# Optimization experiments

Measured on AMD Instinct MI355X. Metric: run time of the kernel, lower is better.

Reference implementation:

```python
import jax, jax.numpy as jnp
import numpy as np

K = 1024  # num_embeddings
D = 256   # embedding_dim
COMMIT = 0.25

def setup_inputs() -> dict:
    key = jax.random.key(0)
    k1, k2 = jax.random.split(key)
    z = jax.random.normal(k1, (32, 256, 32, 32), dtype=jnp.float32)
    # matches nn.Embedding init uniform_(-1/K, 1/K)
    emb = jax.random.uniform(k2, (K, D), dtype=jnp.float32, minval=-1.0 / K, maxval=1.0 / K)
    return {"z": z, "emb": emb}

def reference(z, emb):
    B, C, H, W = z.shape
    zp = jnp.transpose(z, (0, 2, 3, 1))            # (B,H,W,C)
    z_flat = zp.reshape(-1, C)                      # (N,D)
    # squared euclidean distances (N,K)
    d = (jnp.sum(z_flat * z_flat, axis=1, keepdims=True)
         + jnp.sum(emb * emb, axis=1)
         - 2.0 * z_flat @ emb.T)
    idx = jnp.argmin(d, axis=1)                     # (N,)
    quantized_flat = emb[idx]                       # gather == one-hot @ emb
    quantized = quantized_flat.reshape(zp.shape)    # (B,H,W,C)
    e_latent_loss = jnp.mean((jax.lax.stop_gradient(quantized) - zp) ** 2)
    q_latent_loss = jnp.mean((quantized - jax.lax.stop_gradient(zp)) ** 2)
    loss = q_latent_loss + COMMIT * e_latent_loss
    # straight-through estimator
    quantized_st = zp + jax.lax.stop_gradient(quantized - zp)
    # perplexity: avg one-hot probs == normalized counts
    N = z_flat.shape[0]
    counts = jnp.zeros((K,), dtype=jnp.float32).at[idx].add(1.0)
    avg_probs = counts / N
    perplexity = jnp.exp(-jnp.sum(avg_probs * jnp.log(avg_probs + 1e-10)))
    out = jnp.transpose(quantized_st, (0, 3, 1, 2))  # (B,C,H,W)
    return (out, loss, perplexity)
```

## Files before the change

### kernel.cpp

```cpp
#include <hip/hip_runtime.h>
#include <math.h>

#define KC 1024
#define DD 256
#define NROWS 32768
#define NELEM 8388608

typedef _Float16 f16;
typedef __attribute__((ext_vector_type(8))) _Float16 f16x8;
typedef __attribute__((ext_vector_type(16))) float f32x16;

__global__ void vq_prep_kernel(const float* __restrict__ emb, f16* __restrict__ emb_h,
                               float* __restrict__ c_sq, int* __restrict__ counts,
                               float* __restrict__ loss_acc) {
    const int tid = threadIdx.x;
    const int gt = blockIdx.x * 256 + tid;
    if (gt < KC) counts[gt] = 0;
    if (gt == 0) *loss_acc = 0.0f;
    {
        int k = blockIdx.x * 4 + (tid >> 6);
        int lane = tid & 63;
        float4 v = *(const float4*)(emb + (size_t)k * DD + lane * 4);
        float s = v.x * v.x + v.y * v.y + v.z * v.z + v.w * v.w;
        #pragma unroll
        for (int off = 32; off > 0; off >>= 1) s += __shfl_down(s, off);
        if (lane == 0) c_sq[k] = s;
    }
    if (gt < 32768) {
        int code = gt & 1023;
        int kg = gt >> 10;
        const float* p = emb + (size_t)code * DD + kg * 8;
        float4 v0 = *(const float4*)p;
        float4 v1 = *(const float4*)(p + 4);
        f16x8 h;
        h[0] = (f16)v0.x; h[1] = (f16)v0.y; h[2] = (f16)v0.z; h[3] = (f16)v0.w;
        h[4] = (f16)v1.x; h[5] = (f16)v1.y; h[6] = (f16)v1.z; h[7] = (f16)v1.w;
        *(f16x8*)(emb_h + (size_t)gt * 8) = h;
    }
}

__device__ __forceinline__ void upd(float& bv, int& bi, float v, int i) {
    if (v < bv) { bv = v; bi = i; }
}

__global__ __launch_bounds__(256, 3)
void vq_dist_kernel(const float* __restrict__ z, const float* __restrict__ emb,
                    const f16* __restrict__ emb_h, const float* __restrict__ c_sq,
                    int* __restrict__ counts, float* __restrict__ out,
                    float* __restrict__ loss_acc) {
    __shared__ __align__(16) f16 smem[64 * 264];
    __shared__ float bl_v[4][64];
    __shared__ int bl_i[4][64];
    __shared__ int idx_s[64];
    __shared__ float wsum[4];

    const int tid = threadIdx.x;
    const int n0 = blockIdx.x * 64;
    const int b = n0 >> 10;
    const int hw0 = n0 & 1023;

    {
        const int r = tid & 63;
        const int kq = tid >> 6;
        const float* zp = z + (size_t)b * (DD * 1024) + hw0 + r;
        #pragma unroll
        for (int it = 0; it < 8; ++it) {
            int kg = kq * 8 + it;
            f16x8 hv;
            #pragma unroll
            for (int j = 0; j < 8; ++j) hv[j] = (f16)zp[(size_t)(kg * 8 + j) * 1024];
            *(f16x8*)&smem[(kg * 64 + r) * 8] = hv;
        }
    }
    __syncthreads();

    const int m = tid & 31;
    const int h = (tid >> 5) & 1;
    const int w = tid >> 6;

    float bv[32];
    int bi[32];
    #pragma unroll
    for (int s = 0; s < 32; ++s) { bv[s] = 3.0e38f; bi[s] = 0; }

    for (int chunk = 0; chunk < 4; ++chunk) {
        const int cb = chunk * 256 + w * 64;
        const f16* ebp = emb_h + (size_t)h * 8192 + (size_t)(cb + m) * 8;

        f32x16 acc00, acc01, acc10, acc11;
        #pragma unroll
        for (int i = 0; i < 16; ++i) { acc00[i] = 0.f; acc01[i] = 0.f; acc10[i] = 0.f; acc11[i] = 0.f; }

        #pragma unroll 4
        for (int ks = 0; ks < 16; ++ks) {
            const f16* za = smem + ks * 1024 + h * 512 + m * 8;
            f16x8 a0 = *(const f16x8*)(za);
            f16x8 a1 = *(const f16x8*)(za + 256);
            f16x8 b0 = *(const f16x8*)(ebp + (size_t)ks * 16384);
            f16x8 b1 = *(const f16x8*)(ebp + (size_t)ks * 16384 + 256);
            acc00 = __builtin_amdgcn_mfma_f32_32x32x16_f16(a0, b0, acc00, 0, 0, 0);
            acc01 = __builtin_amdgcn_mfma_f32_32x32x16_f16(a0, b1, acc01, 0, 0, 0);
            acc10 = __builtin_amdgcn_mfma_f32_32x32x16_f16(a1, b0, acc10, 0, 0, 0);
            acc11 = __builtin_amdgcn_mfma_f32_32x32x16_f16(a1, b1, acc11, 0, 0, 0);
        }

        const int code0 = cb + m;
        const int code1 = cb + 32 + m;
        const float cs0 = c_sq[code0];
        const float cs1 = c_sq[code1];
        #pragma unroll
        for (int reg = 0; reg < 16; ++reg) {
            upd(bv[reg], bi[reg], fmaf(-2.f, acc00[reg], cs0), code0);
            upd(bv[reg], bi[reg], fmaf(-2.f, acc01[reg], cs1), code1);
            upd(bv[16 + reg], bi[16 + reg], fmaf(-2.f, acc10[reg], cs0), code0);
            upd(bv[16 + reg], bi[16 + reg], fmaf(-2.f, acc11[reg], cs1), code1);
        }
    }

    #pragma unroll
    for (int s = 0; s < 32; ++s) {
        float v = bv[s];
        int i = bi[s];
        #pragma unroll
        for (int d = 16; d >= 1; d >>= 1) {
            float ov = __shfl_xor(v, d);
            int oi = __shfl_xor(i, d);
            if (ov < v || (ov == v && oi < i)) { v = ov; i = oi; }
        }
        bv[s] = v; bi[s] = i;
    }
    if (m == 0) {
        #pragma unroll
        for (int s = 0; s < 32; ++s) {
            int rt = s >> 4, reg = s & 15;
            int row = rt * 32 + (reg & 3) + 8 * (reg >> 2) + 4 * h;
            bl_v[w][row] = bv[s];
            bl_i[w][row] = bi[s];
        }
    }
    __syncthreads();

    if (tid < 64) {
        float v = bl_v[0][tid];
        int i = bl_i[0][tid];
        #pragma unroll
        for (int w2 = 1; w2 < 4; ++w2) {
            float ov = bl_v[w2][tid];
            int oi = bl_i[w2][tid];
            if (ov < v || (ov == v && oi < i)) { v = ov; i = oi; }
        }
        idx_s[tid] = i;
        atomicAdd(&counts[i], 1);
    }
    __syncthreads();

    {
        int r = tid >> 2;
        int part = tid & 3;
        const float* ep = emb + (size_t)idx_s[r] * DD + part * 64;
        f16* qrow = smem + r * 264 + part * 64;
        #pragma unroll
        for (int i = 0; i < 8; ++i) {
            float4 v0 = *(const float4*)(ep + i * 8);
            float4 v1 = *(const float4*)(ep + i * 8 + 4);
            f16x8 hv;
            hv[0] = (f16)v0.x; hv[1] = (f16)v0.y; hv[2] = (f16)v0.z; hv[3] = (f16)v0.w;
            hv[4] = (f16)v1.x; hv[5] = (f16)v1.y; hv[6] = (f16)v1.z; hv[7] = (f16)v1.w;
            *(f16x8*)(qrow + i * 8) = hv;
        }
    }
    __syncthreads();

    float acc = 0.f;
    {
        const int lane = tid & 63;
        const size_t base = (size_t)b * (DD * 1024) + hw0 + lane;
        const f16* qr = smem + lane * 264;
        for (int cg = w; cg < 32; cg += 4) {
            f16x8 qv = *(const f16x8*)(qr + cg * 8);
            #pragma unroll
            for (int j = 0; j < 8; ++j) {
                int c = cg * 8 + j;
                size_t a = base + (size_t)c * 1024;
                float q = (float)qv[j];
                float zv = z[a];
                out[a] = q;
                float d = q - zv;
                acc += d * d;
            }
        }
    }
    #pragma unroll
    for (int off = 32; off > 0; off >>= 1) acc += __shfl_down(acc, off);
    if ((tid & 63) == 0) wsum[w] = acc;
    __syncthreads();
    if (tid == 0) atomicAdd(loss_acc, wsum[0] + wsum[1] + wsum[2] + wsum[3]);
}

__global__ void vq_finalize_kernel(const int* __restrict__ counts,
                                   const float* __restrict__ loss_acc,
                                   float* __restrict__ out_tail) {
    __shared__ float wsum[4];
    const int tid = threadIdx.x;
    float s = 0.f;
    #pragma unroll
    for (int k = tid; k < KC; k += 256) {
        float p = (float)counts[k] * (1.0f / (float)NROWS);
        s += p * logf(p + 1e-10f);
    }
    #pragma unroll
    for (int off = 32; off > 0; off >>= 1) s += __shfl_down(s, off);
    const int lane = tid & 63;
    const int w = tid >> 6;
    if (lane == 0) wsum[w] = s;
    __syncthreads();
    if (tid == 0) {
        float ent = wsum[0] + wsum[1] + wsum[2] + wsum[3];
        out_tail[0] = 1.25f * loss_acc[0] * (1.0f / (float)NELEM);
        out_tail[1] = expf(-ent);
    }
}

extern "C" void kernel_launch(void* const* d_in, const int* in_sizes, int n_in,
                              void* d_out, int out_size, void* d_ws, size_t ws_size,
                              hipStream_t stream) {
    const float* z = (const float*)d_in[0];
    const float* emb = (const float*)d_in[1];
    float* out = (float*)d_out;

    char* wsb = (char*)d_ws;
    f16* emb_h = (f16*)wsb;
    float* c_sq = (float*)(wsb + 524288);
    int* counts = (int*)(wsb + 528384);
    float* loss_acc = (float*)(wsb + 532480);

    hipLaunchKernelGGL(vq_prep_kernel, dim3(256), dim3(256), 0, stream,
                       emb, emb_h, c_sq, counts, loss_acc);
    hipLaunchKernelGGL(vq_dist_kernel, dim3(512), dim3(256), 0, stream,
                       z, emb, emb_h, c_sq, counts, out, loss_acc);
    hipLaunchKernelGGL(vq_finalize_kernel, dim3(1), dim3(256), 0, stream,
                       counts, loss_acc, out + NELEM);
}
```

Before: 138.2 us.

## Fuse finalize into main VQ kernel, widen blocks, compute loss from distances

Blocks grow from 256 to 512 threads, so each wave covers 128 codes instead of looping over four chunks, and the separate finalize kernel becomes a last-block-done reduction inside the main kernel. The loss is now taken from the minimum distance plus the per-row |z|^2 gathered during the z load, which removes the second pass over z in the epilogue. The quantized rows are staged in fp32 in shared memory, so the output holds exact embedding values rather than fp16-rounded ones. The risks are lower occupancy from the larger shared-memory footprint, and a loss value computed from fp16 MFMA dot products, which can differ slightly from the exact squared error.

```diff
diff --git a/kernel.cpp b/kernel.cpp
--- a/kernel.cpp
+++ b/kernel.cpp
@@ -12,11 +12,11 @@
 
 __global__ void vq_prep_kernel(const float* __restrict__ emb, f16* __restrict__ emb_h,
                                float* __restrict__ c_sq, int* __restrict__ counts,
-                               float* __restrict__ loss_acc) {
+                               float* __restrict__ loss_acc, unsigned* __restrict__ done) {
     const int tid = threadIdx.x;
     const int gt = blockIdx.x * 256 + tid;
     if (gt < KC) counts[gt] = 0;
-    if (gt == 0) *loss_acc = 0.0f;
+    if (gt == 0) { *loss_acc = 0.0f; *done = 0u; }
     {
         int k = blockIdx.x * 4 + (tid >> 6);
         int lane = tid & 63;
@@ -43,16 +43,22 @@
     if (v < bv) { bv = v; bi = i; }
 }
 
-__global__ __launch_bounds__(256, 3)
-void vq_dist_kernel(const float* __restrict__ z, const float* __restrict__ emb,
+__global__ __launch_bounds__(512, 4)
+void vq_main_kernel(const float* __restrict__ z, const float* __restrict__ emb,
                     const f16* __restrict__ emb_h, const float* __restrict__ c_sq,
-                    int* __restrict__ counts, float* __restrict__ out,
-                    float* __restrict__ loss_acc) {
-    __shared__ __align__(16) f16 smem[64 * 264];
-    __shared__ float bl_v[4][64];
-    __shared__ int bl_i[4][64];
-    __shared__ int idx_s[64];
-    __shared__ float wsum[4];
+                    int* __restrict__ counts, float* __restrict__ loss_acc,
+                    unsigned* __restrict__ done, float* __restrict__ out,
+                    float* __restrict__ out_tail) {
+    __shared__ __align__(16) char smem_raw[66560];
+    __shared__ float bl_v[8][64];
+    __shared__ int   bl_i[8][64];
+    __shared__ float zsq_part[8][64];
+    __shared__ int   idx_s[64];
+    __shared__ float wsum[8];
+    __shared__ int   last_flag;
+
+    f16* z_s = (f16*)smem_raw;
+    float* Qh = (float*)smem_raw;
 
     const int tid = threadIdx.x;
     const int n0 = blockIdx.x * 64;
@@ -63,14 +69,20 @@
         const int r = tid & 63;
         const int kq = tid >> 6;
         const float* zp = z + (size_t)b * (DD * 1024) + hw0 + r;
-        #pragma unroll
-        for (int it = 0; it < 8; ++it) {
-            int kg = kq * 8 + it;
+        float sq = 0.f;
+        #pragma unroll
+        for (int it = 0; it < 4; ++it) {
+            int kg = kq * 4 + it;
             f16x8 hv;
             #pragma unroll
-            for (int j = 0; j < 8; ++j) hv[j] = (f16)zp[(size_t)(kg * 8 + j) * 1024];
-            *(f16x8*)&smem[(kg * 64 + r) * 8] = hv;
-        }
+            for (int j = 0; j < 8; ++j) {
+                float v = zp[(size_t)(kg * 8 + j) * 1024];
+                sq += v * v;
+                hv[j] = (f16)v;
+            }
+            *(f16x8*)&z_s[(kg * 64 + r) * 8] = hv;
+        }
+        zsq_part[kq][r] = sq;
     }
     __syncthreads();
 
@@ -83,8 +95,8 @@
     #pragma unroll
     for (int s = 0; s < 32; ++s) { bv[s] = 3.0e38f; bi[s] = 0; }
 
-    for (int chunk = 0; chunk < 4; ++chunk) {
-        const int cb = chunk * 256 + w * 64;
+    for (int c = 0; c < 2; ++c) {
+        const int cb = w * 128 + c * 64;
         const f16* ebp = emb_h + (size_t)h * 8192 + (size_t)(cb + m) * 8;
 
         f32x16 acc00, acc01, acc10, acc11;
@@ -93,7 +105,7 @@
 
         #pragma unroll 4
         for (int ks = 0; ks < 16; ++ks) {
-            const f16* za = smem + ks * 1024 + h * 512 + m * 8;
+            const f16* za = z_s + (2 * ks + h) * 512 + m * 8;
             f16x8 a0 = *(const f16x8*)(za);
             f16x8 a1 = *(const f16x8*)(za + 256);
             f16x8 b0 = *(const f16x8*)(ebp + (size_t)ks * 16384);
@@ -144,80 +156,75 @@
         float v = bl_v[0][tid];
         int i = bl_i[0][tid];
         #pragma unroll
-        for (int w2 = 1; w2 < 4; ++w2) {
+        for (int w2 = 1; w2 < 8; ++w2) {
             float ov = bl_v[w2][tid];
             int oi = bl_i[w2][tid];
             if (ov < v || (ov == v && oi < i)) { v = ov; i = oi; }
         }
         idx_s[tid] = i;
         atomicAdd(&counts[i], 1);
-    }
-    __syncthreads();
-
-    {
-        int r = tid >> 2;
-        int part = tid & 3;
-        const float* ep = emb + (size_t)idx_s[r] * DD + part * 64;
-        f16* qrow = smem + r * 264 + part * 64;
-        #pragma unroll
-        for (int i = 0; i < 8; ++i) {
-            float4 v0 = *(const float4*)(ep + i * 8);
-            float4 v1 = *(const float4*)(ep + i * 8 + 4);
-            f16x8 hv;
-            hv[0] = (f16)v0.x; hv[1] = (f16)v0.y; hv[2] = (f16)v0.z; hv[3] = (f16)v0.w;
-            hv[4] = (f16)v1.x; hv[5] = (f16)v1.y; hv[6] = (f16)v1.z; hv[7] = (f16)v1.w;
-            *(f16x8*)(qrow + i * 8) = hv;
-        }
-    }
-    __syncthreads();
-
-    float acc = 0.f;
-    {
-        const int lane = tid & 63;
-        const size_t base = (size_t)b * (DD * 1024) + hw0 + lane;
-        const f16* qr = smem + lane * 264;
-        for (int cg = w; cg < 32; cg += 4) {
-            f16x8 qv = *(const f16x8*)(qr + cg * 8);
+        float zq = 0.f;
+        #pragma unroll
+        for (int p = 0; p < 8; ++p) zq += zsq_part[p][tid];
+        float lr = v + zq;
+        #pragma unroll
+        for (int off = 32; off > 0; off >>= 1) lr += __shfl_down(lr, off);
+        if (tid == 0) atomicAdd(loss_acc, lr);
+    }
+    __syncthreads();
+
+    {
+        int r = tid & 63;
+        int part = tid >> 6;
+        const float* ep = emb + (size_t)idx_s[r] * DD + part * 32;
+        float* qrow = Qh + r * 260 + part * 32;
+        #pragma unroll
+        for (int g = 0; g < 8; ++g)
+            *(float4*)(qrow + g * 4) = *(const float4*)(ep + g * 4);
+    }
+    __syncthreads();
+
+    {
+        int r = tid & 63;
+        const float* qr = Qh + r * 260;
+        const size_t base = (size_t)b * (DD * 1024) + hw0 + r;
+        #pragma unroll
+        for (int g = 0; g < 8; ++g) {
+            int c0 = w * 32 + g * 4;
+            float4 v = *(const float4*)(qr + c0);
+            out[base + (size_t)c0 * 1024] = v.x;
+            out[base + (size_t)(c0 + 1) * 1024] = v.y;
+            out[base + (size_t)(c0 + 2) * 1024] = v.z;
+            out[base + (size_t)(c0 + 3) * 1024] = v.w;
+        }
+    }
+
+    __syncthreads();
+    if (tid == 0) {
+        __threadfence();
+        last_flag = (atomicAdd(done, 1u) == 511u) ? 1 : 0;
+    }
+    __syncthreads();
+    if (last_flag) {
+        __threadfence();
+        float s = 0.f;
+        for (int k = tid; k < KC; k += 512) {
+            int cnt = atomicAdd(&counts[k], 0);
+            float p = (float)cnt * (1.0f / (float)NROWS);
+            s += p * logf(p + 1e-10f);
+        }
+        #pragma unroll
+        for (int off = 32; off > 0; off >>= 1) s += __shfl_down(s, off);
+        if ((tid & 63) == 0) wsum[w] = s;
+        __syncthreads();
+        if (tid == 0) {
+            float ent = 0.f;
             #pragma unroll
-            for (int j = 0; j < 8; ++j) {
-                int c = cg * 8 + j;
-                size_t a = base + (size_t)c * 1024;
-                float q = (float)qv[j];
-                float zv = z[a];
-                out[a] = q;
-                float d = q - zv;
-                acc += d * d;
-            }
-        }
-    }
-    #pragma unroll
-    for (int off = 32; off > 0; off >>= 1) acc += __shfl_down(acc, off);
-    if ((tid & 63) == 0) wsum[w] = acc;
-    __syncthreads();
-    if (tid == 0) atomicAdd(loss_acc, wsum[0] + wsum[1] + wsum[2] + wsum[3]);
-}
-
-__global__ void vq_finalize_kernel(const int* __restrict__ counts,
-                                   const float* __restrict__ loss_acc,
-                                   float* __restrict__ out_tail) {
-    __shared__ float wsum[4];
-    const int tid = threadIdx.x;
-    float s = 0.f;
-    #pragma unroll
-    for (int k = tid; k < KC; k += 256) {
-        float p = (float)counts[k] * (1.0f / (float)NROWS);
-        s += p * logf(p + 1e-10f);
-    }
-    #pragma unroll
-    for (int off = 32; off > 0; off >>= 1) s += __shfl_down(s, off);
-    const int lane = tid & 63;
-    const int w = tid >> 6;
-    if (lane == 0) wsum[w] = s;
-    __syncthreads();
-    if (tid == 0) {
-        float ent = wsum[0] + wsum[1] + wsum[2] + wsum[3];
-        out_tail[0] = 1.25f * loss_acc[0] * (1.0f / (float)NELEM);
-        out_tail[1] = expf(-ent);
+            for (int p = 0; p < 8; ++p) ent += wsum[p];
+            float ls = atomicAdd(loss_acc, 0.0f);
+            out_tail[0] = 1.25f * ls * (1.0f / (float)NELEM);
+            out_tail[1] = expf(-ent);
+        }
     }
 }
 
@@ -233,11 +240,10 @@
     float* c_sq = (float*)(wsb + 524288);
     int* counts = (int*)(wsb + 528384);
     float* loss_acc = (float*)(wsb + 532480);
+    unsigned* done = (unsigned*)(wsb + 532484);
 
     hipLaunchKernelGGL(vq_prep_kernel, dim3(256), dim3(256), 0, stream,
-                       emb, emb_h, c_sq, counts, loss_acc);
-    hipLaunchKernelGGL(vq_dist_kernel, dim3(512), dim3(256), 0, stream,
-                       z, emb, emb_h, c_sq, counts, out, loss_acc);
-    hipLaunchKernelGGL(vq_finalize_kernel, dim3(1), dim3(256), 0, stream,
-                       counts, loss_acc, out + NELEM);
-}
+                       emb, emb_h, c_sq, counts, loss_acc, done);
+    hipLaunchKernelGGL(vq_main_kernel, dim3(512), dim3(512), 0, stream,
+                       z, emb, emb_h, c_sq, counts, loss_acc, done, out, out + NELEM);
+}
```

After: 150.8 us. +9.1%, slower.
